# Performance work log

Hardware: AMD Instinct MI355X
Metric: run time of the kernel (lower is better)

Reference implementation:

```python
import math
import jax, jax.numpy as jnp
import numpy as np

N_TOKENS = 32768
N_TYPES = 21
D_MODEL = 1024
N_SEQS = 64


def setup_inputs() -> dict:
    key = jax.random.key(0)
    k1, k2, k3, k4 = jax.random.split(key, 4)
    x = jax.random.normal(k1, (N_TOKENS, N_TYPES), dtype=jnp.float32)
    # nn.Linear(n_types, d_model): weight [d_model, n_types], bias [d_model]
    W = jax.random.normal(k2, (D_MODEL, N_TYPES), dtype=jnp.float32) / math.sqrt(N_TYPES)
    b = jax.random.normal(k3, (D_MODEL,), dtype=jnp.float32) * 0.01
    # sorted segment ids -> ragged batch of N_SEQS sequences
    batch = jnp.sort(jax.random.randint(k4, (N_TOKENS,), 0, N_SEQS, dtype=jnp.int64))
    return {"x": x, "W": W, "b": b, "batch": batch}


def _position_encoding(max_len, d_model, dtype):
    pos = jnp.arange(max_len, dtype=jnp.float32)[:, None]          # [L,1]
    div = jnp.exp(jnp.arange(0, d_model, 2, dtype=jnp.float32) * (-math.log(10000.0) / d_model))
    ang = pos * div                                                 # [L, d/2]
    pe = jnp.zeros((max_len, d_model), dtype=jnp.float32)
    pe = pe.at[:, 0::2].set(jnp.sin(ang)).at[:, 1::2].set(jnp.cos(ang))
    return pe.astype(dtype)


def reference(x, W, b, batch):
    d_model = W.shape[0]
    # Linear projection + sqrt(d_model) scale
    h = (jnp.einsum('nt,dt->nd', x, W) + b) * math.sqrt(d_model)    # [N, d_model]

    # pad_batch: relabel via unique ids, compute per-token position within its
    # sequence, and scatter into a padded [n_seqs, max_len, d_model] tensor.
    bnp = np.asarray(batch)
    _, inv, counts = np.unique(bnp, return_inverse=True, return_counts=True)
    n_seqs = counts.shape[0]
    max_len = int(counts.max())
    offsets = np.concatenate([np.zeros(1, dtype=np.int64), np.cumsum(counts)[:-1]])
    pos = np.arange(bnp.shape[0], dtype=np.int64) - offsets[inv]    # position within sequence

    padded = jnp.zeros((n_seqs, max_len, d_model), dtype=h.dtype)
    padded = padded.at[jnp.asarray(inv), jnp.asarray(pos)].set(h)

    # mask: True where valid token (original returns ~pad_mask)
    mask = jnp.arange(max_len)[None, :] < jnp.asarray(counts)[:, None]

    pe = _position_encoding(max_len, d_model, h.dtype)              # [L, d_model]
    out = padded + pe[None, :, :]
    return (out, mask)
```

## Files before the change

kernel.cpp:

```cpp
#include <hip/hip_runtime.h>
#include <hip/hip_bf16.h>
#include <math.h>

typedef float f4 __attribute__((ext_vector_type(4)));
typedef float f32x4 __attribute__((ext_vector_type(4)));
typedef short bf16x8 __attribute__((ext_vector_type(8)));

__device__ inline unsigned short f2bf(float f) {
  unsigned int u = __builtin_bit_cast(unsigned int, f);
  unsigned int r = (u + 0x7FFFu + ((u >> 16) & 1u)) >> 16;
  return (unsigned short)r;
}

__global__ __launch_bounds__(256) void setup_kernel(
    const int* __restrict__ batch, int n, const float* __restrict__ W,
    int* __restrict__ tables, unsigned short* __restrict__ wbf) {
  int t = threadIdx.x;

  if (blockIdx.x != 0) {
    int r = (blockIdx.x - 1) * 256 + t;
    const float* wr = W + r * 21;
    unsigned short* wo = wbf + r * 32;
#pragma unroll
    for (int k = 0; k < 21; ++k) wo[k] = f2bf(wr[k]);
#pragma unroll
    for (int k = 21; k < 32; ++k) wo[k] = 0;
    return;
  }

  __shared__ int samp[256];
  __shared__ int csum[64];
  __shared__ int fine[64];
  __shared__ int sbase[64];
  __shared__ int lbs[65];
  __shared__ int stride_s;
  if (t == 0) stride_s = (batch[n - 1] == 0) ? 2 : 1;
  if (t < 64) { csum[t] = 0; fine[t] = 0; }
  __syncthreads();
  int stride = stride_s;
  int window = (n + 255) >> 8;
  {
    long long idx = (long long)t * window;
    if (idx > n - 1) idx = n - 1;
    samp[t] = batch[idx * stride];
  }
  __syncthreads();
  {
    int v = t >> 2, q = t & 3;
    int c = 0;
#pragma unroll
    for (int i = 0; i < 64; ++i) c += (samp[q * 64 + i] < v) ? 1 : 0;
    atomicAdd(&csum[v], c);
  }
  __syncthreads();
  if (t < 64) {
    int c = csum[t];
    sbase[t] = (c == 0) ? 0 : (c - 1) * window;
  }
  __syncthreads();
  {
    int v = t >> 2, q = t & 3;
    int wpt = (window + 3) >> 2;
    int S = sbase[v];
    int c = 0;
    for (int j = q * wpt; j < (q + 1) * wpt && j < window; ++j) {
      int idx = S + j;
      if (idx < n && batch[(size_t)idx * stride] < v) c++;
    }
    atomicAdd(&fine[v], c);
  }
  __syncthreads();
  if (t < 64) {
    lbs[t] = sbase[t] + fine[t];
    if (t == 0) lbs[64] = n;
  }
  __syncthreads();
  if (t < 64) {
    int cnt = lbs[t + 1] - lbs[t];
    unsigned long long present = __ballot(cnt > 0);
    int seg = __popcll(present & ((1ull << t) - 1ull));
    int nseq = __popcll(present);
    if (cnt > 0) { tables[seg] = lbs[t]; tables[64 + seg] = cnt; }
    if (t >= nseq) { tables[t] = 0; tables[64 + t] = 0; }
  }
}

__global__ __launch_bounds__(256) void embed_kernel(
    const float* __restrict__ x, const unsigned short* __restrict__ wb,
    const float* __restrict__ bias, const int* __restrict__ tables,
    float* __restrict__ out, float* __restrict__ mask,
    int L, int n_tokens) {
  int t = threadIdx.x;
  int lane = t & 63;
  int wv = t >> 6;
  int g = lane >> 4, c = lane & 15;

  int stripe = blockIdx.x >> 2;
  int colGroup = blockIdx.x & 3;
  int base = stripe * 16;

  int s0 = base / L;
  int s0L = s0 * L;
  int Lnext = s0L + L;

  int row_c = base + c;
  int inc_c = (row_c >= Lnext) ? 1 : 0;
  int p_c = row_c - (inc_c ? Lnext : s0L);
  int cnt_c = tables[64 + s0 + inc_c];
  bool valid_c = p_c < cnt_c;
  unsigned long long bal = __ballot(valid_c);
  unsigned int m16 = (unsigned int)(bal & 0xFFFFull);
  int rank_c = __popc(m16 & ((1u << c) - 1u));

  int p0 = base - s0L;
  int cnt0 = tables[64 + s0];
  int tok0 = tables[s0] + (p0 < cnt0 ? p0 : cnt0);
  int tok = tok0 + rank_c;
  if (tok > n_tokens - 1) tok = n_tokens - 1;

  const float* xr = x + (size_t)tok * 21;
  float vvx[8];
#pragma unroll
  for (int j = 0; j < 8; ++j) vvx[j] = 0.f;
  if (g == 0) {
#pragma unroll
    for (int j = 0; j < 8; ++j) vvx[j] = xr[j];
  } else if (g == 1) {
#pragma unroll
    for (int j = 0; j < 8; ++j) vvx[j] = xr[8 + j];
  } else if (g == 2) {
#pragma unroll
    for (int j = 0; j < 5; ++j) vvx[j] = xr[16 + j];
  }
  bf16x8 af;
#pragma unroll
  for (int j = 0; j < 8; ++j) af[j] = (short)f2bf(vvx[j]);

  const float KC = -0.01798894603901599f;
  int cb = colGroup * 256 + wv * 64;
  bf16x8 wfr[4];
  f4 bv4[4];
  float dv0[4], dv1[4];
#pragma unroll
  for (int ct = 0; ct < 4; ++ct) {
    wfr[ct] = *(const bf16x8*)(wb + (size_t)(cb + ct * 16 + c) * 32 + 8 * g);
    int dbase = cb + ct * 16 + 4 * g;
    bv4[ct] = *(const f4*)(bias + dbase);
    int pair0 = dbase >> 1;
    dv0[ct] = __expf(KC * (float)pair0);
    dv1[ct] = __expf(KC * (float)(pair0 + 1));
  }

  float fp = (float)p_c;
  float* po = out + (size_t)(base + c) * 1024;

#pragma unroll
  for (int ct = 0; ct < 4; ++ct) {
    f32x4 acc = {0.f, 0.f, 0.f, 0.f};
    acc = __builtin_amdgcn_mfma_f32_16x16x32_bf16(wfr[ct], af, acc, 0, 0, 0);
    float sv0, cv0, sv1, cv1;
    __sincosf(fp * dv0[ct], &sv0, &cv0);
    __sincosf(fp * dv1[ct], &sv1, &cv1);
    f4 res;
    res[0] = valid_c ? fmaf(acc[0] + bv4[ct][0], 32.f, sv0) : sv0;
    res[1] = valid_c ? fmaf(acc[1] + bv4[ct][1], 32.f, cv0) : cv0;
    res[2] = valid_c ? fmaf(acc[2] + bv4[ct][2], 32.f, sv1) : sv1;
    res[3] = valid_c ? fmaf(acc[3] + bv4[ct][3], 32.f, cv1) : cv1;
    *(f4*)(po + cb + ct * 16 + 4 * g) = res;
  }

  if (colGroup == 0 && t < 16)
    mask[base + t] = ((m16 >> t) & 1) ? 1.0f : 0.0f;
}

extern "C" void kernel_launch(void* const* d_in, const int* in_sizes, int n_in,
                              void* d_out, int out_size, void* d_ws, size_t ws_size,
                              hipStream_t stream) {
  const float* x = (const float*)d_in[0];
  const float* W = (const float*)d_in[1];
  const float* b = (const float*)d_in[2];
  const int* batch = (const int*)d_in[3];
  int n_tokens = in_sizes[3];
  float* out = (float*)d_out;

  int L = out_size / (64 * 1025);
  int totalRows = 64 * L;

  int* tables = (int*)d_ws;
  unsigned short* wbf = (unsigned short*)((char*)d_ws + 1024);

  setup_kernel<<<5, 256, 0, stream>>>(batch, n_tokens, W, tables, wbf);

  int stripes = totalRows / 16;
  embed_kernel<<<stripes * 4, 256, 0, stream>>>(x, wbf, b, tables, out,
                                                out + (size_t)totalRows * 1024,
                                                L, n_tokens);
}
```

Measured before the change: 49.01 us.

## Process four 16-row groups per block and transpose MFMA output layout

Each embed block now covers 64 padded rows instead of 16. It loads the bf16 weight fragments, bias and frequency factors once and reuses them across four row groups, carrying the token offset forward between groups with a popcount. The MFMA operands are swapped so each lane owns one output column and four rows. The lane then computes a single sin or cos per element and issues scalar 4-byte stores instead of 16-byte vector stores. Launch bounds add an occupancy hint. The intent is to cut per-block setup and the grid size, at the cost of four times as many store instructions in a write-bound kernel.

```diff
diff --git a/kernel.cpp b/kernel.cpp
--- a/kernel.cpp
+++ b/kernel.cpp
@@ -85,7 +85,7 @@
   }
 }
 
-__global__ __launch_bounds__(256) void embed_kernel(
+__global__ __launch_bounds__(256, 4) void embed_kernel(
     const float* __restrict__ x, const unsigned short* __restrict__ wb,
     const float* __restrict__ bias, const int* __restrict__ tables,
     float* __restrict__ out, float* __restrict__ mask,
@@ -95,82 +95,96 @@
   int wv = t >> 6;
   int g = lane >> 4, c = lane & 15;
 
-  int stripe = blockIdx.x >> 2;
+  int blk = blockIdx.x >> 2;
   int colGroup = blockIdx.x & 3;
-  int base = stripe * 16;
+  int base = blk * 64;
 
   int s0 = base / L;
   int s0L = s0 * L;
   int Lnext = s0L + L;
-
-  int row_c = base + c;
-  int inc_c = (row_c >= Lnext) ? 1 : 0;
-  int p_c = row_c - (inc_c ? Lnext : s0L);
-  int cnt_c = tables[64 + s0 + inc_c];
-  bool valid_c = p_c < cnt_c;
-  unsigned long long bal = __ballot(valid_c);
-  unsigned int m16 = (unsigned int)(bal & 0xFFFFull);
-  int rank_c = __popc(m16 & ((1u << c) - 1u));
+  int cnt0 = tables[64 + s0];
+  int s1 = s0 + 1; if (s1 > 63) s1 = 63;
+  int cnt1 = tables[64 + s1];
 
   int p0 = base - s0L;
-  int cnt0 = tables[64 + s0];
-  int tok0 = tables[s0] + (p0 < cnt0 ? p0 : cnt0);
-  int tok = tok0 + rank_c;
-  if (tok > n_tokens - 1) tok = n_tokens - 1;
-
-  const float* xr = x + (size_t)tok * 21;
-  float vvx[8];
-#pragma unroll
-  for (int j = 0; j < 8; ++j) vvx[j] = 0.f;
-  if (g == 0) {
-#pragma unroll
-    for (int j = 0; j < 8; ++j) vvx[j] = xr[j];
-  } else if (g == 1) {
-#pragma unroll
-    for (int j = 0; j < 8; ++j) vvx[j] = xr[8 + j];
-  } else if (g == 2) {
-#pragma unroll
-    for (int j = 0; j < 5; ++j) vvx[j] = xr[16 + j];
-  }
-  bf16x8 af;
-#pragma unroll
-  for (int j = 0; j < 8; ++j) af[j] = (short)f2bf(vvx[j]);
+  int tokBase = tables[s0] + (p0 < cnt0 ? p0 : cnt0);
 
   const float KC = -0.01798894603901599f;
   int cb = colGroup * 256 + wv * 64;
   bf16x8 wfr[4];
-  f4 bv4[4];
-  float dv0[4], dv1[4];
+  float bv[4], dv[4];
 #pragma unroll
   for (int ct = 0; ct < 4; ++ct) {
-    wfr[ct] = *(const bf16x8*)(wb + (size_t)(cb + ct * 16 + c) * 32 + 8 * g);
-    int dbase = cb + ct * 16 + 4 * g;
-    bv4[ct] = *(const f4*)(bias + dbase);
-    int pair0 = dbase >> 1;
-    dv0[ct] = __expf(KC * (float)pair0);
-    dv1[ct] = __expf(KC * (float)(pair0 + 1));
-  }
-
-  float fp = (float)p_c;
-  float* po = out + (size_t)(base + c) * 1024;
-
-#pragma unroll
-  for (int ct = 0; ct < 4; ++ct) {
-    f32x4 acc = {0.f, 0.f, 0.f, 0.f};
-    acc = __builtin_amdgcn_mfma_f32_16x16x32_bf16(wfr[ct], af, acc, 0, 0, 0);
-    float sv0, cv0, sv1, cv1;
-    __sincosf(fp * dv0[ct], &sv0, &cv0);
-    __sincosf(fp * dv1[ct], &sv1, &cv1);
-    f4 res;
-    res[0] = valid_c ? fmaf(acc[0] + bv4[ct][0], 32.f, sv0) : sv0;
-    res[1] = valid_c ? fmaf(acc[1] + bv4[ct][1], 32.f, cv0) : cv0;
-    res[2] = valid_c ? fmaf(acc[2] + bv4[ct][2], 32.f, sv1) : sv1;
-    res[3] = valid_c ? fmaf(acc[3] + bv4[ct][3], 32.f, cv1) : cv1;
-    *(f4*)(po + cb + ct * 16 + 4 * g) = res;
-  }
-
-  if (colGroup == 0 && t < 16)
-    mask[base + t] = ((m16 >> t) & 1) ? 1.0f : 0.0f;
+    int col = cb + ct * 16 + c;
+    wfr[ct] = *(const bf16x8*)(wb + (size_t)col * 32 + 8 * g);
+    bv[ct] = bias[col];
+    dv[ct] = __expf(KC * (float)(col >> 1));
+  }
+  bool isOdd = (c & 1) != 0;
+
+#pragma unroll
+  for (int rg = 0; rg < 4; ++rg) {
+    int rbase = base + 16 * rg;
+
+    int row_c = rbase + c;
+    int inc_c = (row_c >= Lnext) ? 1 : 0;
+    int p_c = row_c - (inc_c ? Lnext : s0L);
+    int cnt_c = inc_c ? cnt1 : cnt0;
+    bool v_c = p_c < cnt_c;
+    unsigned long long bal = __ballot(v_c);
+    unsigned int m16 = (unsigned int)(bal & 0xFFFFull);
+    int rank_c = __popc(m16 & ((1u << c) - 1u));
+
+    int tok = tokBase + rank_c;
+    if (tok > n_tokens - 1) tok = n_tokens - 1;
+
+    const float* xr = x + (size_t)tok * 21;
+    float vvx[8];
+#pragma unroll
+    for (int j = 0; j < 8; ++j) vvx[j] = 0.f;
+    if (g == 0) {
+#pragma unroll
+      for (int j = 0; j < 8; ++j) vvx[j] = xr[j];
+    } else if (g == 1) {
+#pragma unroll
+      for (int j = 0; j < 8; ++j) vvx[j] = xr[8 + j];
+    } else if (g == 2) {
+#pragma unroll
+      for (int j = 0; j < 5; ++j) vvx[j] = xr[16 + j];
+    }
+    bf16x8 af;
+#pragma unroll
+    for (int j = 0; j < 8; ++j) af[j] = (short)f2bf(vvx[j]);
+
+    int prow[4], pval[4];
+#pragma unroll
+    for (int j = 0; j < 4; ++j) {
+      int rr = 4 * g + j;
+      int row = rbase + rr;
+      int inc = (row >= Lnext) ? 1 : 0;
+      prow[j] = row - (inc ? Lnext : s0L);
+      pval[j] = (m16 >> rr) & 1;
+    }
+
+#pragma unroll
+    for (int ct = 0; ct < 4; ++ct) {
+      int col = cb + ct * 16 + c;
+      f32x4 acc = {0.f, 0.f, 0.f, 0.f};
+      acc = __builtin_amdgcn_mfma_f32_16x16x32_bf16(af, wfr[ct], acc, 0, 0, 0);
+#pragma unroll
+      for (int j = 0; j < 4; ++j) {
+        float ang = (float)prow[j] * dv[ct];
+        float pe = isOdd ? __cosf(ang) : __sinf(ang);
+        float res = pval[j] ? fmaf(acc[j] + bv[ct], 32.f, pe) : pe;
+        out[(size_t)(rbase + 4 * g + j) * 1024 + col] = res;
+      }
+    }
+
+    if (colGroup == 0 && wv == 0 && g == 0)
+      mask[rbase + c] = v_c ? 1.0f : 0.0f;
+
+    tokBase += __popc(m16);
+  }
 }
 
 extern "C" void kernel_launch(void* const* d_in, const int* in_sizes, int n_in,
@@ -191,8 +205,7 @@
 
   setup_kernel<<<5, 256, 0, stream>>>(batch, n_tokens, W, tables, wbf);
 
-  int stripes = totalRows / 16;
-  embed_kernel<<<stripes * 4, 256, 0, stream>>>(x, wbf, b, tables, out,
-                                                out + (size_t)totalRows * 1024,
-                                                L, n_tokens);
-}
+  int rowBlocks = totalRows / 64;
+  embed_kernel<<<rowBlocks * 4, 256, 0, stream>>>(
+      x, wbf, b, tables, out, out + (size_t)totalRows * 1024, L, n_tokens);
+}
```

Measured after the change: 47.88 us. 2.3% less time.
